# Performance work log

Hardware: AMD Instinct MI355X
Metric: run time of the kernel (lower is better)

## Reference

```python
import jax, jax.numpy as jnp
import numpy as np

NUM_HEADS = 4
KSIZE = 3
PAD = KSIZE // 2


def setup_inputs() -> dict:
    key = jax.random.key(0)
    ks = jax.random.split(key, 7)
    C = 128
    D = H = W = 24
    B = 1
    N = D * H * W
    std = 0.02
    return {
        "x": jax.random.normal(ks[0], (B, N, C), dtype=jnp.float32),
        "Wq": jax.random.normal(ks[1], (C, C), dtype=jnp.float32) * std,
        "bq": jnp.zeros((C,), dtype=jnp.float32),
        "Wkv": jax.random.normal(ks[2], (C, 2 * C), dtype=jnp.float32) * std,
        "bkv": jnp.zeros((2 * C,), dtype=jnp.float32),
        "Wp": jax.random.normal(ks[3], (C, C), dtype=jnp.float32) * std,
        "bp": jnp.zeros((C,), dtype=jnp.float32),
        "D": D,
        "H": H,
        "W": W,
    }


def reference(x, Wq, bq, Wkv, bkv, Wp, bp, D, H, W):
    B, N, C = x.shape
    nh = NUM_HEADS
    hc = C // nh
    scale = hc ** -0.5
    k = KSIZE
    K3 = k * k * k

    xv = x.reshape(B, D, H, W, C)
    # q: (B, D, H, W, nh, hc), pre-scaled
    q = (xv @ Wq + bq).reshape(B, D, H, W, nh, hc) * scale
    # kv: (B, D, H, W, 2, nh, hc)
    kv = (xv @ Wkv + bkv).reshape(B, D, H, W, 2, nh, hc)
    # zero-pad spatial dims (ZeroPad3d with pad_size = k//2)
    kvp = jnp.pad(kv, ((0, 0), (PAD, PAD), (PAD, PAD), (PAD, PAD), (0, 0), (0, 0), (0, 0)))
    # gather 3x3x3 neighborhoods via shifted slices (equivalent to unfold with stride=1)
    # nb: (B, D, H, W, K3, 2, nh, hc)
    nb = jnp.stack(
        [kvp[:, i:i + D, j:j + H, l:l + W]
         for i in range(k) for j in range(k) for l in range(k)],
        axis=4,
    )
    k_nb = nb[..., 0, :, :]  # (B,D,H,W,K3,nh,hc)
    v_nb = nb[..., 1, :, :]
    # per-voxel attention over K3 neighbors
    attn = jnp.einsum("bdhwnc,bdhwknc->bdhwnk", q, k_nb)
    attn = jax.nn.softmax(attn, axis=-1)
    out = jnp.einsum("bdhwnk,bdhwknc->bdhwnc", attn, v_nb)
    out = out.reshape(B, D, H, W, C) @ Wp + bp
    return out.reshape(B, N, C)
```

## Files before the change

### kernel.cpp

```cpp
#include <hip/hip_runtime.h>
#include <math.h>

#define NTOK 13824
#define CCH 128
#define DD3 24
#define SCALE 0.17677669529663687f
#define HSTRIDE 136
#define VOFF (144 * HSTRIDE)

typedef float  f32x4  __attribute__((ext_vector_type(4)));
typedef short  s16x8  __attribute__((ext_vector_type(8)));

__device__ __forceinline__ ushort bf16_rtn(float f) {
    unsigned u = __float_as_uint(f);
    unsigned r = u + 0x7fffu + ((u >> 16) & 1u);
    return (ushort)(r >> 16);
}
__device__ __forceinline__ float bf16_f32(ushort h) {
    return __uint_as_float(((unsigned)h) << 16);
}

#define BSW(n, g) ((n) * 128 + ((((g) ^ ((n) & 7))) << 3))

__global__ __launch_bounds__(256) void qkv_all(
    const float* __restrict__ x,
    const float* __restrict__ Wq, const float* __restrict__ bq,
    const float* __restrict__ Wkv, const float* __restrict__ bkv,
    const float* __restrict__ Wp,
    float* __restrict__ qb, ushort* __restrict__ kvb, ushort* __restrict__ wimg)
{
    __shared__ ushort bsh[2][8192];

    const int t  = threadIdx.x;
    const int y  = blockIdx.y;

    if (y == 5 && blockIdx.x < 16) {
        const int i    = 12288 + blockIdx.x * 256 + t;
        const int seg  = i >> 11;
        const int r    = i & 2047;
        const int n    = r & 63;
        const int k4   = (r >> 6) * 4;
        const int scol = (seg - 6) * 64;
        ushort4 hi, lo;
        float v;
        v = Wp[(k4 + 0) * 128 + scol + n]; hi.x = bf16_rtn(v); lo.x = bf16_rtn(v - bf16_f32(hi.x));
        v = Wp[(k4 + 1) * 128 + scol + n]; hi.y = bf16_rtn(v); lo.y = bf16_rtn(v - bf16_f32(hi.y));
        v = Wp[(k4 + 2) * 128 + scol + n]; hi.z = bf16_rtn(v); lo.z = bf16_rtn(v - bf16_f32(hi.z));
        v = Wp[(k4 + 3) * 128 + scol + n]; hi.w = bf16_rtn(v); lo.w = bf16_rtn(v - bf16_f32(hi.w));
        const int f = seg * 16384 + BSW(n, k4 >> 3) + (k4 & 7);
        *(ushort4*)(wimg + f)        = hi;
        *(ushort4*)(wimg + f + 8192) = lo;
    }

    const float* W;
    int ldw, scol;
    if (y < 2) { W = Wq;  ldw = 128; scol = y * 64; }
    else       { W = Wkv; ldw = 256; scol = (y - 2) * 64; }

    #pragma unroll
    for (int p = 0; p < 8; ++p) {
        const int idx = p * 256 + t;
        const int n   = idx & 63;
        const int k4  = (idx >> 6) * 4;
        ushort4 hi, lo;
        float v;
        v = W[(k4 + 0) * ldw + scol + n]; hi.x = bf16_rtn(v); lo.x = bf16_rtn(v - bf16_f32(hi.x));
        v = W[(k4 + 1) * ldw + scol + n]; hi.y = bf16_rtn(v); lo.y = bf16_rtn(v - bf16_f32(hi.y));
        v = W[(k4 + 2) * ldw + scol + n]; hi.z = bf16_rtn(v); lo.z = bf16_rtn(v - bf16_f32(hi.z));
        v = W[(k4 + 3) * ldw + scol + n]; hi.w = bf16_rtn(v); lo.w = bf16_rtn(v - bf16_f32(hi.w));
        const int e = BSW(n, k4 >> 3) + (k4 & 7);
        *(ushort4*)(&bsh[0][e]) = hi;
        *(ushort4*)(&bsh[1][e]) = lo;
    }

    const int wv = t >> 6, l = t & 63;
    const int lm = l & 15, lk = l >> 4;
    const int row = blockIdx.x * 64 + wv * 16 + lm;
    const int ko  = lk * 8;

    s16x8 ah[4], al[4];
    #pragma unroll
    for (int kb = 0; kb < 4; ++kb) {
        const int k0 = kb * 32;
        const float4 a0 = *(const float4*)(x + row * 128 + k0 + ko);
        const float4 a1 = *(const float4*)(x + row * 128 + k0 + ko + 4);
        const float av[8] = {a0.x, a0.y, a0.z, a0.w, a1.x, a1.y, a1.z, a1.w};
        #pragma unroll
        for (int e = 0; e < 8; ++e) {
            const ushort hh = bf16_rtn(av[e]);
            ah[kb][e] = (short)hh;
            al[kb][e] = (short)bf16_rtn(av[e] - bf16_f32(hh));
        }
    }

    __syncthreads();

    f32x4 acc[4];
    #pragma unroll
    for (int nt = 0; nt < 4; ++nt)
        #pragma unroll
        for (int r = 0; r < 4; ++r) acc[nt][r] = 0.f;

    #pragma unroll
    for (int nt = 0; nt < 4; ++nt) {
        const int n = nt * 16 + lm;
        s16x8 bh[4], bl[4];
        #pragma unroll
        for (int kb = 0; kb < 4; ++kb) {
            const int g = kb * 4 + lk;
            bh[kb] = *(const s16x8*)(&bsh[0][BSW(n, g)]);
            bl[kb] = *(const s16x8*)(&bsh[1][BSW(n, g)]);
        }
        #pragma unroll
        for (int kb = 0; kb < 4; ++kb) {
            acc[nt] = __builtin_amdgcn_mfma_f32_16x16x32_bf16(ah[kb], bh[kb], acc[nt], 0, 0, 0);
            acc[nt] = __builtin_amdgcn_mfma_f32_16x16x32_bf16(ah[kb], bl[kb], acc[nt], 0, 0, 0);
            acc[nt] = __builtin_amdgcn_mfma_f32_16x16x32_bf16(al[kb], bh[kb], acc[nt], 0, 0, 0);
        }
    }

    const int orow0 = blockIdx.x * 64 + wv * 16 + lk * 4;
    #pragma unroll
    for (int nt = 0; nt < 4; ++nt) {
        const int col = y * 64 + nt * 16 + lm;
        if (col < 128) {
            const float b = bq[col];
            #pragma unroll
            for (int r = 0; r < 4; ++r)
                qb[(orow0 + r) * 128 + col] = (acc[nt][r] + b) * SCALE;
        } else {
            const int c2 = col - 128;
            const float b = bkv[c2];
            #pragma unroll
            for (int r = 0; r < 4; ++r)
                kvb[(orow0 + r) * 256 + c2] = bf16_rtn(acc[nt][r] + b);
        }
    }
}

__global__ __launch_bounds__(256) void attn_proj(
    const float* __restrict__ qb, const ushort* __restrict__ kvb,
    const ushort* __restrict__ wimg, const float* __restrict__ bp,
    float* __restrict__ out)
{
    __shared__ ushort smem[2 * VOFF];

    const int t   = threadIdx.x;
    const int bid = blockIdx.x;
    const int wv = t >> 6, l = t & 63;
    const int lm = l & 15, lk = l >> 4;

    const int tw = bid % 6, th = (bid / 6) % 6, td = bid / 36;
    const int d0 = td * 2, h0 = th * 4, w0 = tw * 4;

    const int vox = t >> 3;
    const int q8  = t & 7;
    const int ld = vox >> 4, lh = (vox >> 2) & 3, lw = vox & 3;
    const int n  = ((d0 + ld) * DD3 + (h0 + lh)) * DD3 + (w0 + lw);
    const int choff = q8 * 16;

    #pragma unroll
    for (int p = 0; p < 18; ++p) {
        const int idx = p * 256 + t;
        const int r   = idx >> 5;
        const int c2  = idx & 31;
        const int a = r / 36, bb = (r / 6) % 6, cc = r % 6;
        const int gd = d0 - 1 + a, gh = h0 - 1 + bb, gw = w0 - 1 + cc;
        int4 v = {0, 0, 0, 0};
        if ((unsigned)gd < DD3 && (unsigned)gh < DD3 && (unsigned)gw < DD3) {
            const int n2 = (gd * DD3 + gh) * DD3 + gw;
            v = *(const int4*)(kvb + n2 * 256 + c2 * 8);
        }
        const int dst = (c2 < 16) ? (r * HSTRIDE + c2 * 8)
                                  : (VOFF + r * HSTRIDE + (c2 - 16) * 8);
        *(int4*)(smem + dst) = v;
    }

    float qv[16];
    #pragma unroll
    for (int m = 0; m < 4; ++m) {
        const float4 qq = *(const float4*)(qb + n * 128 + choff + m * 4);
        qv[m * 4 + 0] = qq.x; qv[m * 4 + 1] = qq.y;
        qv[m * 4 + 2] = qq.z; qv[m * 4 + 3] = qq.w;
    }

    __syncthreads();

    const int vbase = (ld * 36 + lh * 6 + lw);
    const ushort* kvoxel = smem + vbase * HSTRIDE + choff;
    const ushort* vvoxel = kvoxel + VOFF;

    float logit[27];
    #pragma unroll
    for (int i = 0; i < 3; ++i)
        #pragma unroll
        for (int j = 0; j < 3; ++j)
            #pragma unroll
            for (int l2 = 0; l2 < 3; ++l2) {
                const int idx = (i * 3 + j) * 3 + l2;
                const ushort* kr = kvoxel + (i * 36 + j * 6 + l2) * HSTRIDE;
                const int4 ka = *(const int4*)(kr);
                const int4 kb2 = *(const int4*)(kr + 8);
                float p = 0.f;
                const int* kwa = (const int*)&ka;
                const int* kwb = (const int*)&kb2;
                #pragma unroll
                for (int m = 0; m < 4; ++m) {
                    const unsigned u = (unsigned)kwa[m];
                    p = fmaf(qv[2 * m],     __uint_as_float(u << 16),         p);
                    p = fmaf(qv[2 * m + 1], __uint_as_float(u & 0xffff0000u), p);
                }
                #pragma unroll
                for (int m = 0; m < 4; ++m) {
                    const unsigned u = (unsigned)kwb[m];
                    p = fmaf(qv[8 + 2 * m],     __uint_as_float(u << 16),         p);
                    p = fmaf(qv[8 + 2 * m + 1], __uint_as_float(u & 0xffff0000u), p);
                }
                p += __shfl_xor(p, 1);
                logit[idx] = p;
            }

    float sden;
    {
        #pragma unroll
        for (int idx = 0; idx < 27; ++idx) logit[idx] = __expf(logit[idx]);
        float t1[14];
        #pragma unroll
        for (int k = 0; k < 13; ++k) t1[k] = logit[2 * k] + logit[2 * k + 1];
        t1[13] = logit[26];
        float t2[7];
        #pragma unroll
        for (int k = 0; k < 7; ++k) t2[k] = t1[2 * k] + t1[2 * k + 1];
        sden = ((t2[0] + t2[1]) + (t2[2] + t2[3])) + ((t2[4] + t2[5]) + t2[6]);
    }
    const float inv = 1.f / sden;

    float acc[16];
    #pragma unroll
    for (int m = 0; m < 16; ++m) acc[m] = 0.f;

    #pragma unroll
    for (int i = 0; i < 3; ++i)
        #pragma unroll
        for (int j = 0; j < 3; ++j)
            #pragma unroll
            for (int l2 = 0; l2 < 3; ++l2) {
                const int idx = (i * 3 + j) * 3 + l2;
                const float p = logit[idx];
                const ushort* vr = vvoxel + (i * 36 + j * 6 + l2) * HSTRIDE;
                const int4 va = *(const int4*)(vr);
                const int4 vb2 = *(const int4*)(vr + 8);
                const int* vwa = (const int*)&va;
                const int* vwb = (const int*)&vb2;
                #pragma unroll
                for (int m = 0; m < 4; ++m) {
                    const unsigned u = (unsigned)vwa[m];
                    acc[2 * m]     = fmaf(p, __uint_as_float(u << 16),         acc[2 * m]);
                    acc[2 * m + 1] = fmaf(p, __uint_as_float(u & 0xffff0000u), acc[2 * m + 1]);
                }
                #pragma unroll
                for (int m = 0; m < 4; ++m) {
                    const unsigned u = (unsigned)vwb[m];
                    acc[8 + 2 * m]     = fmaf(p, __uint_as_float(u << 16),         acc[8 + 2 * m]);
                    acc[8 + 2 * m + 1] = fmaf(p, __uint_as_float(u & 0xffff0000u), acc[8 + 2 * m + 1]);
                }
            }

    __syncthreads();

    const char* wsrc = (const char*)(wimg + 6 * 16384);
    #pragma unroll
    for (int p = 0; p < 16; ++p) {
        const int chunk = (wv * 16 + p) * 1024;
        __builtin_amdgcn_global_load_lds(
            (const __attribute__((address_space(1))) void*)(wsrc + chunk + l * 16),
            (__attribute__((address_space(3))) void*)((char*)smem + chunk),
            16, 0, 0);
    }

    {
        ushort hv[16];
        #pragma unroll
        for (int m = 0; m < 16; ++m) hv[m] = bf16_rtn(acc[m] * inv);
        const int g0 = q8 * 2;
        const int e0 = vox * 128 + (((g0)     ^ (vox & 7)) << 3);
        const int e1 = vox * 128 + (((g0 + 1) ^ (vox & 7)) << 3);
        ushort4 w0 = {hv[0], hv[1], hv[2], hv[3]};
        ushort4 w1 = {hv[4], hv[5], hv[6], hv[7]};
        ushort4 w2 = {hv[8], hv[9], hv[10], hv[11]};
        ushort4 w3 = {hv[12], hv[13], hv[14], hv[15]};
        *(ushort4*)(smem + 32768 + e0)     = w0;
        *(ushort4*)(smem + 32768 + e0 + 4) = w1;
        *(ushort4*)(smem + 32768 + e1)     = w2;
        *(ushort4*)(smem + 32768 + e1 + 4) = w3;
    }
    __syncthreads();

    s16x8 pa[2][4];
    #pragma unroll
    for (int rt2 = 0; rt2 < 2; ++rt2)
        #pragma unroll
        for (int kb = 0; kb < 4; ++kb)
            pa[rt2][kb] = *(const s16x8*)(smem + 32768 + BSW(rt2 * 16 + lm, kb * 4 + lk));

    const int ncol = wv * 32;
    f32x4 acc2[2][2];
    #pragma unroll
    for (int rt2 = 0; rt2 < 2; ++rt2)
        #pragma unroll
        for (int ct = 0; ct < 2; ++ct)
            #pragma unroll
            for (int r = 0; r < 4; ++r) acc2[rt2][ct][r] = 0.f;

    #pragma unroll
    for (int ct = 0; ct < 2; ++ct) {
        const int nc = ncol + ct * 16 + lm;
        const int hb = (nc >= 64) ? 16384 : 0;
        const int nn = nc & 63;
        s16x8 bh[4], bl[4];
        #pragma unroll
        for (int kb = 0; kb < 4; ++kb) {
            const int g = kb * 4 + lk;
            bh[kb] = *(const s16x8*)(smem + hb + BSW(nn, g));
            bl[kb] = *(const s16x8*)(smem + hb + 8192 + BSW(nn, g));
        }
        #pragma unroll
        for (int rt2 = 0; rt2 < 2; ++rt2)
            #pragma unroll
            for (int kb = 0; kb < 4; ++kb) {
                acc2[rt2][ct] = __builtin_amdgcn_mfma_f32_16x16x32_bf16(pa[rt2][kb], bh[kb], acc2[rt2][ct], 0, 0, 0);
                acc2[rt2][ct] = __builtin_amdgcn_mfma_f32_16x16x32_bf16(pa[rt2][kb], bl[kb], acc2[rt2][ct], 0, 0, 0);
            }
    }

    #pragma unroll
    for (int rt2 = 0; rt2 < 2; ++rt2)
        #pragma unroll
        for (int ct = 0; ct < 2; ++ct) {
            const int col = ncol + ct * 16 + lm;
            const float bb = bp[col];
            #pragma unroll
            for (int r = 0; r < 4; ++r) {
                const int vox3 = rt2 * 16 + lk * 4 + r;
                const int ld3 = vox3 >> 4, lh3 = (vox3 >> 2) & 3, lw3 = vox3 & 3;
                const int n3 = ((d0 + ld3) * DD3 + (h0 + lh3)) * DD3 + (w0 + lw3);
                out[n3 * 128 + col] = acc2[rt2][ct][r] + bb;
            }
        }
}

extern "C" void kernel_launch(void* const* d_in, const int* in_sizes, int n_in,
                              void* d_out, int out_size, void* d_ws, size_t ws_size,
                              hipStream_t stream) {
    const float* x   = (const float*)d_in[0];
    const float* Wq  = (const float*)d_in[1];
    const float* bq  = (const float*)d_in[2];
    const float* Wkv = (const float*)d_in[3];
    const float* bkv = (const float*)d_in[4];
    const float* Wp  = (const float*)d_in[5];
    const float* bp  = (const float*)d_in[6];
    float* out = (float*)d_out;

    char* ws = (char*)d_ws;
    float*  qb   = (float*)(ws);
    ushort* kvb  = (ushort*)(ws + 7077888);
    ushort* wimg = (ushort*)(ws + 14155776);

    dim3 g1(NTOK / 64, 6);
    qkv_all<<<g1, 256, 0, stream>>>(x, Wq, bq, Wkv, bkv, Wp, qb, kvb, wimg);
    attn_proj<<<432, 256, 0, stream>>>(qb, kvb, wimg, bp, out);
}
```

Before: 39.32 us.

## Double attn_proj block size to 512 threads, halving per-thread channel work

The attention+projection kernel now launches 512 threads per block. Each voxel gets 16 threads of 8 channels each instead of 8 threads of 16, and dot-product reductions use an extra shuffle step. In the projection GEMM each of the 8 waves computes one 16-column tile instead of two. This spreads the per-block work over more waves to raise latency hiding and shorten each thread's serial chain. The cost is extra shuffles, duplicated B-fragment loads, and more register pressure per CU.

```diff
diff --git a/kernel.cpp b/kernel.cpp
--- a/kernel.cpp
+++ b/kernel.cpp
@@ -138,7 +138,7 @@
     }
 }
 
-__global__ __launch_bounds__(256) void attn_proj(
+__global__ __launch_bounds__(512) void attn_proj(
     const float* __restrict__ qb, const ushort* __restrict__ kvb,
     const ushort* __restrict__ wimg, const float* __restrict__ bp,
     float* __restrict__ out)
@@ -153,15 +153,15 @@
     const int tw = bid % 6, th = (bid / 6) % 6, td = bid / 36;
     const int d0 = td * 2, h0 = th * 4, w0 = tw * 4;
 
-    const int vox = t >> 3;
-    const int q8  = t & 7;
+    const int vox   = t >> 4;
+    const int sub16 = t & 15;
     const int ld = vox >> 4, lh = (vox >> 2) & 3, lw = vox & 3;
     const int n  = ((d0 + ld) * DD3 + (h0 + lh)) * DD3 + (w0 + lw);
-    const int choff = q8 * 16;
-
-    #pragma unroll
-    for (int p = 0; p < 18; ++p) {
-        const int idx = p * 256 + t;
+    const int choff = sub16 * 8;
+
+    #pragma unroll
+    for (int p = 0; p < 9; ++p) {
+        const int idx = p * 512 + t;
         const int r   = idx >> 5;
         const int c2  = idx & 31;
         const int a = r / 36, bb = (r / 6) % 6, cc = r % 6;
@@ -176,9 +176,9 @@
         *(int4*)(smem + dst) = v;
     }
 
-    float qv[16];
-    #pragma unroll
-    for (int m = 0; m < 4; ++m) {
+    float qv[8];
+    #pragma unroll
+    for (int m = 0; m < 2; ++m) {
         const float4 qq = *(const float4*)(qb + n * 128 + choff + m * 4);
         qv[m * 4 + 0] = qq.x; qv[m * 4 + 1] = qq.y;
         qv[m * 4 + 2] = qq.z; qv[m * 4 + 3] = qq.w;
@@ -200,23 +200,16 @@
                 const int idx = (i * 3 + j) * 3 + l2;
                 const ushort* kr = kvoxel + (i * 36 + j * 6 + l2) * HSTRIDE;
                 const int4 ka = *(const int4*)(kr);
-                const int4 kb2 = *(const int4*)(kr + 8);
                 float p = 0.f;
-                const int* kwa = (const int*)&ka;
-                const int* kwb = (const int*)&kb2;
+                const int* kw = (const int*)&ka;
                 #pragma unroll
                 for (int m = 0; m < 4; ++m) {
-                    const unsigned u = (unsigned)kwa[m];
+                    const unsigned u = (unsigned)kw[m];
                     p = fmaf(qv[2 * m],     __uint_as_float(u << 16),         p);
                     p = fmaf(qv[2 * m + 1], __uint_as_float(u & 0xffff0000u), p);
                 }
-                #pragma unroll
-                for (int m = 0; m < 4; ++m) {
-                    const unsigned u = (unsigned)kwb[m];
-                    p = fmaf(qv[8 + 2 * m],     __uint_as_float(u << 16),         p);
-                    p = fmaf(qv[8 + 2 * m + 1], __uint_as_float(u & 0xffff0000u), p);
-                }
                 p += __shfl_xor(p, 1);
+                p += __shfl_xor(p, 2);
                 logit[idx] = p;
             }
 
@@ -235,9 +228,9 @@
     }
     const float inv = 1.f / sden;
 
-    float acc[16];
-    #pragma unroll
-    for (int m = 0; m < 16; ++m) acc[m] = 0.f;
+    float acc[8];
+    #pragma unroll
+    for (int m = 0; m < 8; ++m) acc[m] = 0.f;
 
     #pragma unroll
     for (int i = 0; i < 3; ++i)
@@ -249,29 +242,21 @@
                 const float p = logit[idx];
                 const ushort* vr = vvoxel + (i * 36 + j * 6 + l2) * HSTRIDE;
                 const int4 va = *(const int4*)(vr);
-                const int4 vb2 = *(const int4*)(vr + 8);
-                const int* vwa = (const int*)&va;
-                const int* vwb = (const int*)&vb2;
+                const int* vw = (const int*)&va;
                 #pragma unroll
                 for (int m = 0; m < 4; ++m) {
-                    const unsigned u = (unsigned)vwa[m];
+                    const unsigned u = (unsigned)vw[m];
                     acc[2 * m]     = fmaf(p, __uint_as_float(u << 16),         acc[2 * m]);
                     acc[2 * m + 1] = fmaf(p, __uint_as_float(u & 0xffff0000u), acc[2 * m + 1]);
                 }
-                #pragma unroll
-                for (int m = 0; m < 4; ++m) {
-                    const unsigned u = (unsigned)vwb[m];
-                    acc[8 + 2 * m]     = fmaf(p, __uint_as_float(u << 16),         acc[8 + 2 * m]);
-                    acc[8 + 2 * m + 1] = fmaf(p, __uint_as_float(u & 0xffff0000u), acc[8 + 2 * m + 1]);
-                }
             }
 
     __syncthreads();
 
     const char* wsrc = (const char*)(wimg + 6 * 16384);
     #pragma unroll
-    for (int p = 0; p < 16; ++p) {
-        const int chunk = (wv * 16 + p) * 1024;
+    for (int p = 0; p < 8; ++p) {
+        const int chunk = (wv * 8 + p) * 1024;
         __builtin_amdgcn_global_load_lds(
             (const __attribute__((address_space(1))) void*)(wsrc + chunk + l * 16),
             (__attribute__((address_space(3))) void*)((char*)smem + chunk),
@@ -279,20 +264,16 @@
     }
 
     {
-        ushort hv[16];
-        #pragma unroll
-        for (int m = 0; m < 16; ++m) hv[m] = bf16_rtn(acc[m] * inv);
-        const int g0 = q8 * 2;
-        const int e0 = vox * 128 + (((g0)     ^ (vox & 7)) << 3);
-        const int e1 = vox * 128 + (((g0 + 1) ^ (vox & 7)) << 3);
-        ushort4 w0 = {hv[0], hv[1], hv[2], hv[3]};
-        ushort4 w1 = {hv[4], hv[5], hv[6], hv[7]};
-        ushort4 w2 = {hv[8], hv[9], hv[10], hv[11]};
-        ushort4 w3 = {hv[12], hv[13], hv[14], hv[15]};
-        *(ushort4*)(smem + 32768 + e0)     = w0;
-        *(ushort4*)(smem + 32768 + e0 + 4) = w1;
-        *(ushort4*)(smem + 32768 + e1)     = w2;
-        *(ushort4*)(smem + 32768 + e1 + 4) = w3;
+        int pk[4];
+        #pragma unroll
+        for (int m = 0; m < 4; ++m) {
+            const float e0 = acc[2 * m] * inv;
+            const float e1 = acc[2 * m + 1] * inv;
+            pk[m] = (int)bf16_rtn(e0) | ((int)bf16_rtn(e1) << 16);
+        }
+        int4 w0 = {pk[0], pk[1], pk[2], pk[3]};
+        const int e = vox * 128 + (((sub16) ^ (vox & 7)) << 3);
+        *(int4*)(smem + 32768 + e) = w0;
     }
     __syncthreads();
 
@@ -303,49 +284,43 @@
         for (int kb = 0; kb < 4; ++kb)
             pa[rt2][kb] = *(const s16x8*)(smem + 32768 + BSW(rt2 * 16 + lm, kb * 4 + lk));
 
-    const int ncol = wv * 32;
-    f32x4 acc2[2][2];
+    const int ncol = wv * 16;
+    const int nc   = ncol + lm;
+    const int hb   = (nc >= 64) ? 16384 : 0;
+    const int nn   = nc & 63;
+
+    s16x8 bh[4], bl[4];
+    #pragma unroll
+    for (int kb = 0; kb < 4; ++kb) {
+        const int g = kb * 4 + lk;
+        bh[kb] = *(const s16x8*)(smem + hb + BSW(nn, g));
+        bl[kb] = *(const s16x8*)(smem + hb + 8192 + BSW(nn, g));
+    }
+
+    f32x4 acc2[2];
     #pragma unroll
     for (int rt2 = 0; rt2 < 2; ++rt2)
         #pragma unroll
-        for (int ct = 0; ct < 2; ++ct)
-            #pragma unroll
-            for (int r = 0; r < 4; ++r) acc2[rt2][ct][r] = 0.f;
-
-    #pragma unroll
-    for (int ct = 0; ct < 2; ++ct) {
-        const int nc = ncol + ct * 16 + lm;
-        const int hb = (nc >= 64) ? 16384 : 0;
-        const int nn = nc & 63;
-        s16x8 bh[4], bl[4];
+        for (int r = 0; r < 4; ++r) acc2[rt2][r] = 0.f;
+
+    #pragma unroll
+    for (int rt2 = 0; rt2 < 2; ++rt2)
         #pragma unroll
         for (int kb = 0; kb < 4; ++kb) {
-            const int g = kb * 4 + lk;
-            bh[kb] = *(const s16x8*)(smem + hb + BSW(nn, g));
-            bl[kb] = *(const s16x8*)(smem + hb + 8192 + BSW(nn, g));
-        }
-        #pragma unroll
-        for (int rt2 = 0; rt2 < 2; ++rt2)
-            #pragma unroll
-            for (int kb = 0; kb < 4; ++kb) {
-                acc2[rt2][ct] = __builtin_amdgcn_mfma_f32_16x16x32_bf16(pa[rt2][kb], bh[kb], acc2[rt2][ct], 0, 0, 0);
-                acc2[rt2][ct] = __builtin_amdgcn_mfma_f32_16x16x32_bf16(pa[rt2][kb], bl[kb], acc2[rt2][ct], 0, 0, 0);
-            }
-    }
-
+            acc2[rt2] = __builtin_amdgcn_mfma_f32_16x16x32_bf16(pa[rt2][kb], bh[kb], acc2[rt2], 0, 0, 0);
+            acc2[rt2] = __builtin_amdgcn_mfma_f32_16x16x32_bf16(pa[rt2][kb], bl[kb], acc2[rt2], 0, 0, 0);
+        }
+
+    const int col = ncol + lm;
+    const float bb = bp[col];
     #pragma unroll
     for (int rt2 = 0; rt2 < 2; ++rt2)
         #pragma unroll
-        for (int ct = 0; ct < 2; ++ct) {
-            const int col = ncol + ct * 16 + lm;
-            const float bb = bp[col];
-            #pragma unroll
-            for (int r = 0; r < 4; ++r) {
-                const int vox3 = rt2 * 16 + lk * 4 + r;
-                const int ld3 = vox3 >> 4, lh3 = (vox3 >> 2) & 3, lw3 = vox3 & 3;
-                const int n3 = ((d0 + ld3) * DD3 + (h0 + lh3)) * DD3 + (w0 + lw3);
-                out[n3 * 128 + col] = acc2[rt2][ct][r] + bb;
-            }
+        for (int r = 0; r < 4; ++r) {
+            const int vox3 = rt2 * 16 + lk * 4 + r;
+            const int ld3 = vox3 >> 4, lh3 = (vox3 >> 2) & 3, lw3 = vox3 & 3;
+            const int n3 = ((d0 + ld3) * DD3 + (h0 + lh3)) * DD3 + (w0 + lw3);
+            out[n3 * 128 + col] = acc2[rt2][r] + bb;
         }
 }
 
@@ -368,5 +343,5 @@
 
     dim3 g1(NTOK / 64, 6);
     qkv_all<<<g1, 256, 0, stream>>>(x, Wq, bq, Wkv, bkv, Wp, qb, kvb, wimg);
-    attn_proj<<<432, 256, 0, stream>>>(qb, kvb, wimg, bp, out);
-}
+    attn_proj<<<432, 512, 0, stream>>>(qb, kvb, wimg, bp, out);
+}
```

After: 42.55 us. +8.2%, slower.
